# Performance work log

Hardware: AMD Instinct MI355X
Metric: run time of the kernel (lower is better)

## Reference

```python
import jax, jax.numpy as jnp
import numpy as np

T = 4096          # tokens (batch*seq)
D = 768           # moe_intermediate_size (token hidden dim)
I = 2048          # intermediate_size (FFN inner dim)
E = 8             # num_experts


def setup_inputs() -> dict:
    key = jax.random.key(0)
    k_x, k_p, k_g, k_u, k_d = jax.random.split(key, 5)
    hidden_states = jax.random.normal(k_x, (T, D), dtype=jnp.float32)
    position_index = jax.random.randint(k_p, (T,), 0, E, dtype=jnp.int64)
    behavior_index = jnp.zeros((T,), dtype=jnp.int64)  # unused (behavior_injection=False)
    s = 0.02
    # torch Linear weight layout: [out_features, in_features]
    gate_w = jax.random.normal(k_g, (E, I, D), dtype=jnp.float32) * s
    up_w = jax.random.normal(k_u, (E, I, D), dtype=jnp.float32) * s
    down_w = jax.random.normal(k_d, (E, D, I), dtype=jnp.float32) * s
    return {
        "hidden_states": hidden_states,
        "position_index": position_index,
        "behavior_index": behavior_index,
        "gate_w": gate_w,
        "up_w": up_w,
        "down_w": down_w,
    }


def reference(hidden_states, position_index, behavior_index, gate_w, up_w, down_w):
    # Sparse MoE dispatch: each token routed to exactly one expert by position_index.
    # Dropout rate is 0.0 (eval) -> identity. behavior_injection=False -> behavior_index unused.
    num_experts = gate_w.shape[0]
    out = jnp.zeros_like(hidden_states)
    for e in range(num_experts):  # structural loop over fixed expert count
        mask = (position_index == e)[:, None]          # [T, 1]
        g = hidden_states @ gate_w[e].T                 # [T, I]
        u = hidden_states @ up_w[e].T                   # [T, I]
        y = (jax.nn.silu(g) * u) @ down_w[e].T          # [T, D]
        out = out + jnp.where(mask, y, 0.0)             # scatter-combine
    return out
```

## Files before the change

### kernel.cpp

```cpp
#include <hip/hip_runtime.h>
#include <hip/hip_bf16.h>

#define T_TOK 4096
#define DDIM  768
#define IDIM  2048
#define NEXP  8

typedef __attribute__((ext_vector_type(8))) short  bfrag;
typedef __attribute__((ext_vector_type(4))) float  ffrag;

static __device__ __forceinline__ unsigned short f2bf(float f) {
    union { float f; unsigned u; } v; v.f = f;
    unsigned r = v.u + 0x7FFFu + ((v.u >> 16) & 1u);
    return (unsigned short)(r >> 16);
}

__global__ void k_hist(const int* __restrict__ pos, int* __restrict__ ws_i) {
    int t = blockIdx.x * blockDim.x + threadIdx.x;
    if (t < T_TOK) atomicAdd(&ws_i[pos[t]], 1);
}

__global__ void k_scan(int* __restrict__ ws_i) {
    if (threadIdx.x == 0) {
        int s = 0;
        for (int e = 0; e < NEXP; ++e) { ws_i[16 + e] = s; ws_i[8 + e] = s; s += ws_i[e]; }
        ws_i[16 + NEXP] = s;
    }
}

__global__ void k_perm(const int* __restrict__ pos, int* __restrict__ ws_i,
                       int* __restrict__ perm) {
    int t = blockIdx.x * blockDim.x + threadIdx.x;
    if (t < T_TOK) {
        int e = pos[t];
        int p = atomicAdd(&ws_i[8 + e], 1);
        perm[p] = t;
    }
}

__global__ void k_gather(const float* __restrict__ x, const int* __restrict__ perm,
                         unsigned short* __restrict__ xg) {
    int p = blockIdx.x;
    int tok = perm[p];
    int j = threadIdx.x * 4;
    const float4 v = *reinterpret_cast<const float4*>(x + (size_t)tok * DDIM + j);
    uint2 o;
    o.x = f2bf(v.x) | ((unsigned)f2bf(v.y) << 16);
    o.y = f2bf(v.z) | ((unsigned)f2bf(v.w) << 16);
    *reinterpret_cast<uint2*>(xg + (size_t)p * DDIM + j) = o;
}

__launch_bounds__(256, 2)
__global__ void k_gemm1(const unsigned short* __restrict__ xg,
                        const float* __restrict__ gate_w,
                        const float* __restrict__ up_w,
                        unsigned short* __restrict__ hg,
                        const int* __restrict__ ws_i) {
    const int e   = blockIdx.z;
    const int cnt = ws_i[e];
    const int m0  = blockIdx.y * 128;
    if (m0 >= cnt) return;
    const int off = ws_i[16 + e];
    const int n0  = blockIdx.x * 64;

    const int tid  = threadIdx.x;
    const int lane = tid & 63;
    const int wave = tid >> 6;
    const int wm   = wave & 1;
    const int wn   = wave >> 1;

    __shared__ __align__(16) unsigned short lsA[128 * 56];
    __shared__ __align__(16) unsigned short lsG[64 * 56];
    __shared__ __align__(16) unsigned short lsU[64 * 56];

    const float* gate_e = gate_w + (size_t)e * IDIM * DDIM;
    const float* up_e   = up_w   + (size_t)e * IDIM * DDIM;

    ffrag accG[4][2], accU[4][2];
    const ffrag fz = {0.f, 0.f, 0.f, 0.f};
    for (int mi = 0; mi < 4; ++mi)
        for (int ni = 0; ni < 2; ++ni) { accG[mi][ni] = fz; accU[mi][ni] = fz; }

    for (int kt = 0; kt < DDIM / 32; ++kt) {
        const int k0 = kt * 32;
        #pragma unroll
        for (int i = 0; i < 2; ++i) {
            int c = tid + i * 256;
            int row = c >> 2, q = c & 3;
            int grow = off + m0 + row; if (grow > T_TOK - 1) grow = T_TOK - 1;
            const uint4 v = *reinterpret_cast<const uint4*>(xg + (size_t)grow * DDIM + k0 + q * 8);
            *reinterpret_cast<uint4*>(&lsA[row * 56 + q * 8]) = v;
        }
        #pragma unroll
        for (int i = 0; i < 4; ++i) {
            int f   = tid + i * 256;
            int mat = f >> 9;
            int c   = f & 511;
            int row = c >> 3, q = c & 7;
            const float* src = mat ? up_e : gate_e;
            const float4 v = *reinterpret_cast<const float4*>(src + (size_t)(n0 + row) * DDIM + k0 + q * 4);
            uint2 o;
            o.x = f2bf(v.x) | ((unsigned)f2bf(v.y) << 16);
            o.y = f2bf(v.z) | ((unsigned)f2bf(v.w) << 16);
            unsigned short* dst = mat ? lsU : lsG;
            *reinterpret_cast<uint2*>(&dst[row * 56 + q * 4]) = o;
        }
        __syncthreads();

        const int koff = (lane >> 4) * 8;
        const int rsel = lane & 15;
        bfrag a[4], bg[2], bu[2];
        #pragma unroll
        for (int mi = 0; mi < 4; ++mi)
            a[mi] = *reinterpret_cast<const bfrag*>(&lsA[(wm * 64 + mi * 16 + rsel) * 56 + koff]);
        #pragma unroll
        for (int ni = 0; ni < 2; ++ni) {
            bg[ni] = *reinterpret_cast<const bfrag*>(&lsG[(wn * 32 + ni * 16 + rsel) * 56 + koff]);
            bu[ni] = *reinterpret_cast<const bfrag*>(&lsU[(wn * 32 + ni * 16 + rsel) * 56 + koff]);
        }
        #pragma unroll
        for (int mi = 0; mi < 4; ++mi)
            #pragma unroll
            for (int ni = 0; ni < 2; ++ni) {
                accG[mi][ni] = __builtin_amdgcn_mfma_f32_16x16x32_bf16(a[mi], bg[ni], accG[mi][ni], 0, 0, 0);
                accU[mi][ni] = __builtin_amdgcn_mfma_f32_16x16x32_bf16(a[mi], bu[ni], accU[mi][ni], 0, 0, 0);
            }
        __syncthreads();
    }

    const int colb  = lane & 15;
    const int rquad = (lane >> 4) * 4;
    #pragma unroll
    for (int mi = 0; mi < 4; ++mi)
        #pragma unroll
        for (int ni = 0; ni < 2; ++ni) {
            int n = n0 + wn * 32 + ni * 16 + colb;
            #pragma unroll
            for (int r = 0; r < 4; ++r) {
                int ml = wm * 64 + mi * 16 + rquad + r;
                if (m0 + ml < cnt) {
                    float g = accG[mi][ni][r];
                    float u = accU[mi][ni][r];
                    float h = (g / (1.0f + __expf(-g))) * u;
                    hg[(size_t)(off + m0 + ml) * IDIM + n] = f2bf(h);
                }
            }
        }
}

__launch_bounds__(256, 2)
__global__ void k_gemm2(const unsigned short* __restrict__ hg,
                        const float* __restrict__ down_w,
                        float* __restrict__ out,
                        const int* __restrict__ ws_i,
                        const int* __restrict__ perm) {
    const int e   = blockIdx.z;
    const int cnt = ws_i[e];
    const int m0  = blockIdx.y * 128;
    if (m0 >= cnt) return;
    const int off = ws_i[16 + e];
    const int n0  = blockIdx.x * 64;

    const int tid  = threadIdx.x;
    const int lane = tid & 63;
    const int wave = tid >> 6;
    const int wm   = wave & 1;
    const int wn   = wave >> 1;

    __shared__ __align__(16) unsigned short lsA[128 * 56];
    __shared__ __align__(16) unsigned short lsB[64 * 56];

    const float* down_e = down_w + (size_t)e * DDIM * IDIM;

    ffrag acc[4][2];
    const ffrag fz = {0.f, 0.f, 0.f, 0.f};
    for (int mi = 0; mi < 4; ++mi)
        for (int ni = 0; ni < 2; ++ni) acc[mi][ni] = fz;

    for (int kt = 0; kt < IDIM / 32; ++kt) {
        const int k0 = kt * 32;
        #pragma unroll
        for (int i = 0; i < 2; ++i) {
            int c = tid + i * 256;
            int row = c >> 2, q = c & 3;
            int grow = off + m0 + row; if (grow > T_TOK - 1) grow = T_TOK - 1;
            const uint4 v = *reinterpret_cast<const uint4*>(hg + (size_t)grow * IDIM + k0 + q * 8);
            *reinterpret_cast<uint4*>(&lsA[row * 56 + q * 8]) = v;
        }
        #pragma unroll
        for (int i = 0; i < 2; ++i) {
            int c = tid + i * 256;
            int row = c >> 3, q = c & 7;
            const float4 v = *reinterpret_cast<const float4*>(down_e + (size_t)(n0 + row) * IDIM + k0 + q * 4);
            uint2 o;
            o.x = f2bf(v.x) | ((unsigned)f2bf(v.y) << 16);
            o.y = f2bf(v.z) | ((unsigned)f2bf(v.w) << 16);
            *reinterpret_cast<uint2*>(&lsB[row * 56 + q * 4]) = o;
        }
        __syncthreads();

        const int koff = (lane >> 4) * 8;
        const int rsel = lane & 15;
        bfrag a[4], b[2];
        #pragma unroll
        for (int mi = 0; mi < 4; ++mi)
            a[mi] = *reinterpret_cast<const bfrag*>(&lsA[(wm * 64 + mi * 16 + rsel) * 56 + koff]);
        #pragma unroll
        for (int ni = 0; ni < 2; ++ni)
            b[ni] = *reinterpret_cast<const bfrag*>(&lsB[(wn * 32 + ni * 16 + rsel) * 56 + koff]);
        #pragma unroll
        for (int mi = 0; mi < 4; ++mi)
            #pragma unroll
            for (int ni = 0; ni < 2; ++ni)
                acc[mi][ni] = __builtin_amdgcn_mfma_f32_16x16x32_bf16(a[mi], b[ni], acc[mi][ni], 0, 0, 0);
        __syncthreads();
    }

    const int colb  = lane & 15;
    const int rquad = (lane >> 4) * 4;
    #pragma unroll
    for (int mi = 0; mi < 4; ++mi)
        #pragma unroll
        for (int ni = 0; ni < 2; ++ni) {
            int n = n0 + wn * 32 + ni * 16 + colb;
            #pragma unroll
            for (int r = 0; r < 4; ++r) {
                int ml = wm * 64 + mi * 16 + rquad + r;
                if (m0 + ml < cnt) {
                    int tok = perm[off + m0 + ml];
                    out[(size_t)tok * DDIM + n] = acc[mi][ni][r];
                }
            }
        }
}

extern "C" void kernel_launch(void* const* d_in, const int* in_sizes, int n_in,
                              void* d_out, int out_size, void* d_ws, size_t ws_size,
                              hipStream_t stream) {
    const float* x      = (const float*)d_in[0];
    const int*   pos    = (const int*)d_in[1];
    const float* gate_w = (const float*)d_in[3];
    const float* up_w   = (const float*)d_in[4];
    const float* down_w = (const float*)d_in[5];
    float* out = (float*)d_out;

    char* ws = (char*)d_ws;
    int* ws_i = (int*)ws;
    int* perm = (int*)(ws + 1024);
    unsigned short* xg = (unsigned short*)(ws + 32768);
    unsigned short* hg = (unsigned short*)(ws + (8u << 20));

    hipMemsetAsync(ws, 0, 256, stream);
    k_hist<<<dim3(T_TOK / 256), dim3(256), 0, stream>>>(pos, ws_i);
    k_scan<<<dim3(1), dim3(64), 0, stream>>>(ws_i);
    k_perm<<<dim3(T_TOK / 256), dim3(256), 0, stream>>>(pos, ws_i, perm);
    k_gather<<<dim3(T_TOK), dim3(192), 0, stream>>>(x, perm, xg);

    dim3 g1(IDIM / 64, 32, NEXP);
    k_gemm1<<<g1, dim3(256), 0, stream>>>(xg, gate_w, up_w, hg, ws_i);
    dim3 g2(DDIM / 64, 32, NEXP);
    k_gemm2<<<g2, dim3(256), 0, stream>>>(hg, down_w, out, ws_i, perm);
}
```

Before: 353.8 us.

## Register-prefetch GEMM tiles, split-K down projection with atomics, fuse routing kernels

Both GEMM kernels now load the next K-slice of activations and weights into registers while MFMAs run on the current LDS tile, a simple software pipeline meant to hide global-load latency. The down-projection GEMM is split four ways along K and accumulates into a zeroed output with float atomics, so more blocks are in flight when per-expert token counts give few M tiles. The histogram, scan and permutation kernels are merged into one single-block kernel using shared-memory atomics, which cuts launches. Costs are an extra output memset, atomic contention on output rows, and non-deterministic summation order.

Measured after the change: 305.4 us. 13.7% less time.

```diff
diff --git a/kernel.cpp b/kernel.cpp
--- a/kernel.cpp
+++ b/kernel.cpp
@@ -15,26 +15,33 @@
     return (unsigned short)(r >> 16);
 }
 
-__global__ void k_hist(const int* __restrict__ pos, int* __restrict__ ws_i) {
-    int t = blockIdx.x * blockDim.x + threadIdx.x;
-    if (t < T_TOK) atomicAdd(&ws_i[pos[t]], 1);
-}
-
-__global__ void k_scan(int* __restrict__ ws_i) {
-    if (threadIdx.x == 0) {
+static __device__ __forceinline__ unsigned cvt2(float x, float y) {
+    return (unsigned)f2bf(x) | ((unsigned)f2bf(y) << 16);
+}
+
+__global__ void k_sort(const int* __restrict__ pos, int* __restrict__ ws_i,
+                       int* __restrict__ perm) {
+    __shared__ int hist[NEXP], cursor[NEXP];
+    const int tid = threadIdx.x;
+    if (tid < NEXP) hist[tid] = 0;
+    __syncthreads();
+    for (int i = tid; i < T_TOK; i += 1024)
+        atomicAdd(&hist[pos[i]], 1);
+    __syncthreads();
+    if (tid == 0) {
         int s = 0;
-        for (int e = 0; e < NEXP; ++e) { ws_i[16 + e] = s; ws_i[8 + e] = s; s += ws_i[e]; }
+        for (int e = 0; e < NEXP; ++e) {
+            cursor[e] = s;
+            ws_i[e] = hist[e];
+            ws_i[16 + e] = s;
+            s += hist[e];
+        }
         ws_i[16 + NEXP] = s;
     }
-}
-
-__global__ void k_perm(const int* __restrict__ pos, int* __restrict__ ws_i,
-                       int* __restrict__ perm) {
-    int t = blockIdx.x * blockDim.x + threadIdx.x;
-    if (t < T_TOK) {
-        int e = pos[t];
-        int p = atomicAdd(&ws_i[8 + e], 1);
-        perm[p] = t;
+    __syncthreads();
+    for (int i = tid; i < T_TOK; i += 1024) {
+        int p = atomicAdd(&cursor[pos[i]], 1);
+        perm[p] = i;
     }
 }
 
@@ -45,8 +52,8 @@
     int j = threadIdx.x * 4;
     const float4 v = *reinterpret_cast<const float4*>(x + (size_t)tok * DDIM + j);
     uint2 o;
-    o.x = f2bf(v.x) | ((unsigned)f2bf(v.y) << 16);
-    o.y = f2bf(v.z) | ((unsigned)f2bf(v.w) << 16);
+    o.x = cvt2(v.x, v.y);
+    o.y = cvt2(v.z, v.w);
     *reinterpret_cast<uint2*>(xg + (size_t)p * DDIM + j) = o;
 }
 
@@ -73,42 +80,61 @@
     __shared__ __align__(16) unsigned short lsG[64 * 56];
     __shared__ __align__(16) unsigned short lsU[64 * 56];
 
-    const float* gate_e = gate_w + (size_t)e * IDIM * DDIM;
-    const float* up_e   = up_w   + (size_t)e * IDIM * DDIM;
+    const float* gate_e = gate_w + (size_t)e * (IDIM * DDIM);
+    const float* up_e   = up_w   + (size_t)e * (IDIM * DDIM);
+
+    const int ar = tid >> 2;
+    const int aq = tid & 3;
+    const int br = tid >> 3;
+    const int bq = tid & 7;
+
+    int g0 = off + m0 + ar;      if (g0 > T_TOK - 1) g0 = T_TOK - 1;
+    int g1 = off + m0 + ar + 64; if (g1 > T_TOK - 1) g1 = T_TOK - 1;
+    const unsigned short* a0p = xg + (size_t)g0 * DDIM + aq * 8;
+    const unsigned short* a1p = xg + (size_t)g1 * DDIM + aq * 8;
+    const float* gp0 = gate_e + (size_t)(n0 + br)      * DDIM + bq * 4;
+    const float* gp1 = gate_e + (size_t)(n0 + br + 32) * DDIM + bq * 4;
+    const float* up0 = up_e   + (size_t)(n0 + br)      * DDIM + bq * 4;
+    const float* up1 = up_e   + (size_t)(n0 + br + 32) * DDIM + bq * 4;
+
+    uint4  pa0 = *reinterpret_cast<const uint4*>(a0p);
+    uint4  pa1 = *reinterpret_cast<const uint4*>(a1p);
+    float4 pg0 = *reinterpret_cast<const float4*>(gp0);
+    float4 pg1 = *reinterpret_cast<const float4*>(gp1);
+    float4 pu0 = *reinterpret_cast<const float4*>(up0);
+    float4 pu1 = *reinterpret_cast<const float4*>(up1);
 
     ffrag accG[4][2], accU[4][2];
     const ffrag fz = {0.f, 0.f, 0.f, 0.f};
     for (int mi = 0; mi < 4; ++mi)
         for (int ni = 0; ni < 2; ++ni) { accG[mi][ni] = fz; accU[mi][ni] = fz; }
 
+    const int koff = (lane >> 4) * 8;
+    const int rsel = lane & 15;
+
     for (int kt = 0; kt < DDIM / 32; ++kt) {
-        const int k0 = kt * 32;
-        #pragma unroll
-        for (int i = 0; i < 2; ++i) {
-            int c = tid + i * 256;
-            int row = c >> 2, q = c & 3;
-            int grow = off + m0 + row; if (grow > T_TOK - 1) grow = T_TOK - 1;
-            const uint4 v = *reinterpret_cast<const uint4*>(xg + (size_t)grow * DDIM + k0 + q * 8);
-            *reinterpret_cast<uint4*>(&lsA[row * 56 + q * 8]) = v;
-        }
-        #pragma unroll
-        for (int i = 0; i < 4; ++i) {
-            int f   = tid + i * 256;
-            int mat = f >> 9;
-            int c   = f & 511;
-            int row = c >> 3, q = c & 7;
-            const float* src = mat ? up_e : gate_e;
-            const float4 v = *reinterpret_cast<const float4*>(src + (size_t)(n0 + row) * DDIM + k0 + q * 4);
-            uint2 o;
-            o.x = f2bf(v.x) | ((unsigned)f2bf(v.y) << 16);
-            o.y = f2bf(v.z) | ((unsigned)f2bf(v.w) << 16);
-            unsigned short* dst = mat ? lsU : lsG;
-            *reinterpret_cast<uint2*>(&dst[row * 56 + q * 4]) = o;
-        }
+        *reinterpret_cast<uint4*>(&lsA[ar * 56 + aq * 8])        = pa0;
+        *reinterpret_cast<uint4*>(&lsA[(ar + 64) * 56 + aq * 8]) = pa1;
+        { uint2 o; o.x = cvt2(pg0.x, pg0.y); o.y = cvt2(pg0.z, pg0.w);
+          *reinterpret_cast<uint2*>(&lsG[br * 56 + bq * 4]) = o; }
+        { uint2 o; o.x = cvt2(pg1.x, pg1.y); o.y = cvt2(pg1.z, pg1.w);
+          *reinterpret_cast<uint2*>(&lsG[(br + 32) * 56 + bq * 4]) = o; }
+        { uint2 o; o.x = cvt2(pu0.x, pu0.y); o.y = cvt2(pu0.z, pu0.w);
+          *reinterpret_cast<uint2*>(&lsU[br * 56 + bq * 4]) = o; }
+        { uint2 o; o.x = cvt2(pu1.x, pu1.y); o.y = cvt2(pu1.z, pu1.w);
+          *reinterpret_cast<uint2*>(&lsU[(br + 32) * 56 + bq * 4]) = o; }
         __syncthreads();
 
-        const int koff = (lane >> 4) * 8;
-        const int rsel = lane & 15;
+        if (kt < DDIM / 32 - 1) {
+            const int kb = (kt + 1) * 32;
+            pa0 = *reinterpret_cast<const uint4*>(a0p + kb);
+            pa1 = *reinterpret_cast<const uint4*>(a1p + kb);
+            pg0 = *reinterpret_cast<const float4*>(gp0 + kb);
+            pg1 = *reinterpret_cast<const float4*>(gp1 + kb);
+            pu0 = *reinterpret_cast<const float4*>(up0 + kb);
+            pu1 = *reinterpret_cast<const float4*>(up1 + kb);
+        }
+
         bfrag a[4], bg[2], bu[2];
         #pragma unroll
         for (int mi = 0; mi < 4; ++mi)
@@ -154,7 +180,8 @@
                         float* __restrict__ out,
                         const int* __restrict__ ws_i,
                         const int* __restrict__ perm) {
-    const int e   = blockIdx.z;
+    const int e     = blockIdx.z & 7;
+    const int split = blockIdx.z >> 3;
     const int cnt = ws_i[e];
     const int m0  = blockIdx.y * 128;
     if (m0 >= cnt) return;
@@ -170,37 +197,50 @@
     __shared__ __align__(16) unsigned short lsA[128 * 56];
     __shared__ __align__(16) unsigned short lsB[64 * 56];
 
-    const float* down_e = down_w + (size_t)e * DDIM * IDIM;
+    const float* down_e = down_w + (size_t)e * (DDIM * IDIM);
+
+    const int ar = tid >> 2;
+    const int aq = tid & 3;
+    const int br = tid >> 3;
+    const int bq = tid & 7;
+
+    int g0 = off + m0 + ar;      if (g0 > T_TOK - 1) g0 = T_TOK - 1;
+    int g1 = off + m0 + ar + 64; if (g1 > T_TOK - 1) g1 = T_TOK - 1;
+    const unsigned short* a0p = hg + (size_t)g0 * IDIM + split * 512 + aq * 8;
+    const unsigned short* a1p = hg + (size_t)g1 * IDIM + split * 512 + aq * 8;
+    const float* bp0 = down_e + (size_t)(n0 + br)      * IDIM + split * 512 + bq * 4;
+    const float* bp1 = down_e + (size_t)(n0 + br + 32) * IDIM + split * 512 + bq * 4;
+
+    uint4  pa0 = *reinterpret_cast<const uint4*>(a0p);
+    uint4  pa1 = *reinterpret_cast<const uint4*>(a1p);
+    float4 pb0 = *reinterpret_cast<const float4*>(bp0);
+    float4 pb1 = *reinterpret_cast<const float4*>(bp1);
 
     ffrag acc[4][2];
     const ffrag fz = {0.f, 0.f, 0.f, 0.f};
     for (int mi = 0; mi < 4; ++mi)
         for (int ni = 0; ni < 2; ++ni) acc[mi][ni] = fz;
 
-    for (int kt = 0; kt < IDIM / 32; ++kt) {
-        const int k0 = kt * 32;
-        #pragma unroll
-        for (int i = 0; i < 2; ++i) {
-            int c = tid + i * 256;
-            int row = c >> 2, q = c & 3;
-            int grow = off + m0 + row; if (grow > T_TOK - 1) grow = T_TOK - 1;
-            const uint4 v = *reinterpret_cast<const uint4*>(hg + (size_t)grow * IDIM + k0 + q * 8);
-            *reinterpret_cast<uint4*>(&lsA[row * 56 + q * 8]) = v;
-        }
-        #pragma unroll
-        for (int i = 0; i < 2; ++i) {
-            int c = tid + i * 256;
-            int row = c >> 3, q = c & 7;
-            const float4 v = *reinterpret_cast<const float4*>(down_e + (size_t)(n0 + row) * IDIM + k0 + q * 4);
-            uint2 o;
-            o.x = f2bf(v.x) | ((unsigned)f2bf(v.y) << 16);
-            o.y = f2bf(v.z) | ((unsigned)f2bf(v.w) << 16);
-            *reinterpret_cast<uint2*>(&lsB[row * 56 + q * 4]) = o;
-        }
+    const int koff = (lane >> 4) * 8;
+    const int rsel = lane & 15;
+
+    for (int kt = 0; kt < 16; ++kt) {
+        *reinterpret_cast<uint4*>(&lsA[ar * 56 + aq * 8])        = pa0;
+        *reinterpret_cast<uint4*>(&lsA[(ar + 64) * 56 + aq * 8]) = pa1;
+        { uint2 o; o.x = cvt2(pb0.x, pb0.y); o.y = cvt2(pb0.z, pb0.w);
+          *reinterpret_cast<uint2*>(&lsB[br * 56 + bq * 4]) = o; }
+        { uint2 o; o.x = cvt2(pb1.x, pb1.y); o.y = cvt2(pb1.z, pb1.w);
+          *reinterpret_cast<uint2*>(&lsB[(br + 32) * 56 + bq * 4]) = o; }
         __syncthreads();
 
-        const int koff = (lane >> 4) * 8;
-        const int rsel = lane & 15;
+        if (kt < 15) {
+            const int kb = (kt + 1) * 32;
+            pa0 = *reinterpret_cast<const uint4*>(a0p + kb);
+            pa1 = *reinterpret_cast<const uint4*>(a1p + kb);
+            pb0 = *reinterpret_cast<const float4*>(bp0 + kb);
+            pb1 = *reinterpret_cast<const float4*>(bp1 + kb);
+        }
+
         bfrag a[4], b[2];
         #pragma unroll
         for (int mi = 0; mi < 4; ++mi)
@@ -228,7 +268,7 @@
                 int ml = wm * 64 + mi * 16 + rquad + r;
                 if (m0 + ml < cnt) {
                     int tok = perm[off + m0 + ml];
-                    out[(size_t)tok * DDIM + n] = acc[mi][ni][r];
+                    unsafeAtomicAdd(&out[(size_t)tok * DDIM + n], acc[mi][ni][r]);
                 }
             }
         }
@@ -250,14 +290,12 @@
     unsigned short* xg = (unsigned short*)(ws + 32768);
     unsigned short* hg = (unsigned short*)(ws + (8u << 20));
 
-    hipMemsetAsync(ws, 0, 256, stream);
-    k_hist<<<dim3(T_TOK / 256), dim3(256), 0, stream>>>(pos, ws_i);
-    k_scan<<<dim3(1), dim3(64), 0, stream>>>(ws_i);
-    k_perm<<<dim3(T_TOK / 256), dim3(256), 0, stream>>>(pos, ws_i, perm);
+    (void)hipMemsetAsync(d_out, 0, (size_t)out_size * sizeof(float), stream);
+    k_sort<<<dim3(1), dim3(1024), 0, stream>>>(pos, ws_i, perm);
     k_gather<<<dim3(T_TOK), dim3(192), 0, stream>>>(x, perm, xg);
 
     dim3 g1(IDIM / 64, 32, NEXP);
     k_gemm1<<<g1, dim3(256), 0, stream>>>(xg, gate_w, up_w, hg, ws_i);
-    dim3 g2(DDIM / 64, 32, NEXP);
+    dim3 g2(DDIM / 64, 32, NEXP * 4);
     k_gemm2<<<g2, dim3(256), 0, stream>>>(hg, down_w, out, ws_i, perm);
 }
```
